# Kernel tuning notes

Hardware: AMD Instinct MI355X
Metric: run time of the kernel (lower is better)

The kernel has to match this reference:

```python
import jax, jax.numpy as jnp
import numpy as np
from jax import lax

EPS = 1e-5
DN = ('NCDHW', 'OIDHW', 'NCDHW')


def _instance_norm(x, w, b):
    # normalize over spatial dims per (batch, channel); biased variance like torch
    mu = jnp.mean(x, axis=(2, 3, 4), keepdims=True)
    var = jnp.mean((x - mu) ** 2, axis=(2, 3, 4), keepdims=True)
    xn = (x - mu) * lax.rsqrt(var + EPS)
    return xn * w[None, :, None, None, None] + b[None, :, None, None, None]


def _conv1x1(x, w, b):
    # w: [Cout, Cin]
    y = jnp.einsum('bcdhw,oc->bodhw', x, w)
    return y + b[None, :, None, None, None]


def _dwconv3(x, w, b):
    # depthwise 3x3x3, padding 1; w: [C, 1, 3, 3, 3]
    y = lax.conv_general_dilated(x, w, (1, 1, 1), 'SAME',
                                 dimension_numbers=DN,
                                 feature_group_count=w.shape[0])
    return y + b[None, :, None, None, None]


def setup_inputs() -> dict:
    key = jax.random.key(0)
    ks = jax.random.split(key, 8)
    C, half = 64, 32
    B, D, H, W = 1, 96, 96, 96
    s1 = 1.0 / np.sqrt(C)          # fan_in of 1x1 conv
    s3 = 1.0 / np.sqrt(27.0)       # fan_in of depthwise 3x3x3
    return {
        'x': jax.random.normal(ks[0], (B, C, D, H, W), jnp.float32),
        'norm_w': jnp.ones((C,), jnp.float32),
        'norm_b': jnp.zeros((C,), jnp.float32),
        'in_proj_w': jax.random.normal(ks[1], (C, C), jnp.float32) * s1,
        'in_proj_b': jnp.zeros((C,), jnp.float32),
        'conv_ssm_w': jax.random.normal(ks[2], (half, 1, 3, 3, 3), jnp.float32) * s3,
        'conv_ssm_b': jnp.zeros((half,), jnp.float32),
        'mamba_w': jax.random.normal(ks[3], (half, 1, 3, 3, 3), jnp.float32) * s3,
        'mamba_b': jnp.zeros((half,), jnp.float32),
        'conv_sym_w': jax.random.normal(ks[4], (half, 1, 3, 3, 3), jnp.float32) * s3,
        'conv_sym_b': jnp.zeros((half,), jnp.float32),
        'out_proj_w': jax.random.normal(ks[5], (C, C), jnp.float32) * s1,
        'out_proj_b': jnp.zeros((C,), jnp.float32),
    }


def reference(x, norm_w, norm_b, in_proj_w, in_proj_b,
              conv_ssm_w, conv_ssm_b, mamba_w, mamba_b,
              conv_sym_w, conv_sym_b, out_proj_w, out_proj_b):
    residual = x
    xp = _conv1x1(_instance_norm(x, norm_w, norm_b), in_proj_w, in_proj_b)
    half = xp.shape[1] // 2
    x1, x2 = xp[:, :half], xp[:, half:]
    # SSM branch (TriDirectionalMamba fallback = depthwise conv3)
    x1 = _dwconv3(jax.nn.silu(_dwconv3(x1, conv_ssm_w, conv_ssm_b)), mamba_w, mamba_b)
    # symmetric conv branch
    x2 = jax.nn.silu(_dwconv3(x2, conv_sym_w, conv_sym_b))
    y = _conv1x1(jnp.concatenate([x1, x2], axis=1), out_proj_w, out_proj_b)
    return y + residual
```

## Files before the change

### kernel.cpp

```cpp
#include <hip/hip_runtime.h>

typedef unsigned short u16;
typedef unsigned int u32;
typedef short bf16x8 __attribute__((ext_vector_type(8)));
typedef float f32x16 __attribute__((ext_vector_type(16)));
typedef u16 u16x8 __attribute__((ext_vector_type(8)));

#define DIM 96
#define PLANE (DIM*DIM)
#define S 884736
#define C 64
#define HALF 32
#define PARTS 16
#define EPS 1e-5f

#define RPAD 104
#define LROWS 18
#define LBUF (8 + LROWS*RPAD)

#define MFMA32(a,b,c) __builtin_amdgcn_mfma_f32_32x32x16_bf16(a,b,c,0,0,0)

__device__ __forceinline__ u16 f2bf(float f) {
  u32 u = __builtin_bit_cast(u32, f);
  return (u16)((u + 0x7FFFu + ((u >> 16) & 1u)) >> 16);
}
__device__ __forceinline__ float bf2f(u16 h) {
  return __builtin_bit_cast(float, (u32)h << 16);
}
__device__ __forceinline__ u32 cvt_pk_bf16(float lo, float hi) {
  u32 r;
  asm("v_cvt_pk_bf16_f32 %0, %1, %2" : "=v"(r) : "v"(lo), "v"(hi));
  return r;
}
__device__ __forceinline__ float silu(float v) { return v / (1.f + __expf(-v)); }
__device__ __forceinline__ u16x8 zero8() {
  u16x8 z;
  #pragma unroll
  for (int i = 0; i < 8; ++i) z[i] = 0;
  return z;
}

__global__ __launch_bounds__(256) void k1_stats(const float* __restrict__ x,
                                                u16* __restrict__ xb,
                                                float* __restrict__ psum,
                                                float* __restrict__ psq) {
  const int bid = blockIdx.x;
  const int ch = bid / PARTS, part = bid % PARTS;
  const int chunk = S / PARTS;
  const size_t base = (size_t)ch * S + (size_t)part * chunk;
  const float4* p = (const float4*)(x + base);
  ushort4* xb4 = (ushort4*)(xb + base);
  const int n4 = chunk / 4;
  float s = 0.f, q = 0.f;
  for (int i = threadIdx.x; i < n4; i += 256) {
    float4 v = p[i];
    s += (v.x + v.y) + (v.z + v.w);
    q += (v.x * v.x + v.y * v.y) + (v.z * v.z + v.w * v.w);
    union { u32 u[2]; ushort4 v4; } o;
    o.u[0] = cvt_pk_bf16(v.x, v.y);
    o.u[1] = cvt_pk_bf16(v.z, v.w);
    xb4[i] = o.v4;
  }
  #pragma unroll
  for (int off = 32; off > 0; off >>= 1) {
    s += __shfl_down(s, off);
    q += __shfl_down(q, off);
  }
  __shared__ float ls[4], lq[4];
  const int wid = threadIdx.x >> 6, lane = threadIdx.x & 63;
  if (lane == 0) { ls[wid] = s; lq[wid] = q; }
  __syncthreads();
  if (threadIdx.x == 0) {
    psum[bid] = (ls[0] + ls[1]) + (ls[2] + ls[3]);
    psq[bid]  = (lq[0] + lq[1]) + (lq[2] + lq[3]);
  }
}

__global__ __launch_bounds__(64) void k1b_prep(const float* __restrict__ psum,
    const float* __restrict__ psq,
    const float* __restrict__ norm_w, const float* __restrict__ norm_b,
    const float* __restrict__ in_w, const float* __restrict__ in_b,
    const float* __restrict__ out_w,
    u16* __restrict__ Wp, float* __restrict__ biasp, u16* __restrict__ Wo) {
  __shared__ float a_s[C], b2_s[C];
  const int t = threadIdx.x;
  float s = 0.f, q = 0.f;
  for (int i = 0; i < PARTS; ++i) { s += psum[t * PARTS + i]; q += psq[t * PARTS + i]; }
  const float inv = 1.f / (float)S;
  const float mu = s * inv;
  const float var = q * inv - mu * mu;
  const float rsig = rsqrtf(var + EPS);
  const float a = norm_w[t] * rsig;
  const float b2 = norm_b[t] - mu * a;
  a_s[t] = a; b2_s[t] = b2;
  __syncthreads();
  float bp = in_b[t];
  for (int c = 0; c < C; ++c) {
    const float w = in_w[t * C + c];
    Wp[t * C + c] = f2bf(w * a_s[c]);
    bp += b2_s[c] * w;
    Wo[t * C + c] = f2bf(out_w[t * C + c]);
  }
  biasp[t] = bp;
}

__global__ __launch_bounds__(256) void k2_mfma(const u16* __restrict__ xb,
    const u16* __restrict__ Wp, const float* __restrict__ biasp,
    u16* __restrict__ xp) {
  const int lane = threadIdx.x & 63, wid = threadIdx.x >> 6;
  const int n = lane & 31, hf = lane >> 5;
  const int v0 = blockIdx.x * 256 + wid * 64;
  bf16x8 A[2][4];
  #pragma unroll
  for (int t = 0; t < 2; ++t)
    #pragma unroll
    for (int s = 0; s < 4; ++s)
      A[t][s] = *(const bf16x8*)(Wp + (t * 32 + n) * C + s * 16 + hf * 8);

  f32x16 accE[2], accO[2];
  #pragma unroll
  for (int t = 0; t < 2; ++t)
    #pragma unroll
    for (int r = 0; r < 16; ++r) {
      const float b = biasp[t * 32 + (r & 3) + 8 * (r >> 2) + 4 * hf];
      accE[t][r] = b; accO[t][r] = b;
    }

  #pragma unroll
  for (int s = 0; s < 4; ++s) {
    union { u16 u[8]; bf16x8 v; } BE, BO;
    #pragma unroll
    for (int j = 0; j < 8; ++j) {
      const u32 xv = *(const u32*)(xb + (size_t)(s * 16 + hf * 8 + j) * S + v0 + 2 * n);
      BE.u[j] = (u16)(xv & 0xFFFFu); BO.u[j] = (u16)(xv >> 16);
    }
    #pragma unroll
    for (int t = 0; t < 2; ++t) {
      accE[t] = MFMA32(A[t][s], BE.v, accE[t]);
      accO[t] = MFMA32(A[t][s], BO.v, accO[t]);
    }
  }
  #pragma unroll
  for (int t = 0; t < 2; ++t)
    #pragma unroll
    for (int r = 0; r < 16; ++r) {
      const int o = t * 32 + (r & 3) + 8 * (r >> 2) + 4 * hf;
      *(u32*)(xp + (size_t)o * S + v0 + 2 * n) = cvt_pk_bf16(accE[t][r], accO[t][r]);
    }
}

__device__ __forceinline__ void fma3(float* __restrict__ a,
    const float* __restrict__ r, float t0, float t1, float t2) {
  #pragma unroll
  for (int i = 0; i < 8; ++i) a[i] = fmaf(t0, r[i], a[i]);
  #pragma unroll
  for (int i = 0; i < 8; ++i) a[i] = fmaf(t1, r[i + 1], a[i]);
  #pragma unroll
  for (int i = 0; i < 8; ++i) a[i] = fmaf(t2, r[i + 2], a[i]);
}

template<bool SILU, int DCHUNKT>
__global__ __launch_bounds__(192) void dwconv(const u16* __restrict__ srcA,
    const float* __restrict__ kwA, const float* __restrict__ bA,
    u16* __restrict__ dstA,
    const float* __restrict__ kwB, const float* __restrict__ bB,
    u16* __restrict__ dstB) {
  __shared__ u16 lds[2][LBUF];
  const int c = blockIdx.z;
  const u16* src = srcA + (size_t)c * S;
  u16* dst; const float* kwp; float bias;
  if (c < HALF) { dst = dstA + (size_t)c * S;          kwp = kwA + c * 27;          bias = bA[c]; }
  else          { dst = dstB + (size_t)(c - HALF) * S; kwp = kwB + (c - HALF) * 27; bias = bB[c - HALF]; }
  float kw[27];
  #pragma unroll
  for (int i = 0; i < 27; ++i) kw[i] = kwp[i];

  const int tx = threadIdx.x, ty = threadIdx.y;
  const int tid = ty * 12 + tx;
  const int w8 = tx * 8;
  const int h0 = blockIdx.x * 16;
  const int d0 = blockIdx.y * DCHUNKT;

  if (tid < 38) {
    const int b = tid / 19, k = tid % 19;
    *(u16x8*)&lds[b][RPAD * k] = zero8();
  }

  const int s_row0 = tid / 12, s_cc0 = tid % 12;
  const int s_row1 = (192 + tid) / 12, s_cc1 = (192 + tid) % 12;
  const bool has2 = tid < 24;
  const int s_h0 = h0 - 1 + s_row0;
  const int s_h1 = h0 - 1 + s_row1;
  const bool h0ok = (unsigned)s_h0 < DIM;
  const bool h1ok = has2 && ((unsigned)s_h1 < DIM);
  u16x8 vs0, vs1;

  #define STAGE_LOAD(DD) { \
    vs0 = zero8(); vs1 = zero8(); \
    if (((unsigned)(DD) < DIM) && h0ok) \
      vs0 = *(const u16x8*)(src + (size_t)(DD) * PLANE + s_h0 * DIM + s_cc0 * 8); \
    if (((unsigned)(DD) < DIM) && h1ok) \
      vs1 = *(const u16x8*)(src + (size_t)(DD) * PLANE + s_h1 * DIM + s_cc1 * 8); }

  #define STAGE_WRITE(WB) { \
    *(u16x8*)&lds[WB][8 + s_row0 * RPAD + s_cc0 * 8] = vs0; \
    if (has2) *(u16x8*)&lds[WB][8 + s_row1 * RPAD + s_cc1 * 8] = vs1; }

  float r0[10], r1[10], r2[10];
  float A[8], B[8], o8[8];

  #define LOADROW(R, ROWI, RB) { \
    const u16* _lb = &lds[RB][8 + (ROWI) * RPAD + w8]; \
    const u16x8 _m = *(const u16x8*)_lb; \
    const u16 _lo = _lb[-1], _hi = _lb[8]; \
    R[0] = bf2f(_lo); \
    _Pragma("unroll") \
    for (int i = 0; i < 8; ++i) R[1 + i] = bf2f(_m[i]); \
    R[9] = bf2f(_hi); }

  #define LOADROWS(RB) { LOADROW(r0, ty, RB); LOADROW(r1, ty + 1, RB); LOADROW(r2, ty + 2, RB); }

  #define CBLK(ACC, K0) { \
    fma3(ACC, r0, kw[(K0) + 0], kw[(K0) + 1], kw[(K0) + 2]); \
    fma3(ACC, r1, kw[(K0) + 3], kw[(K0) + 4], kw[(K0) + 5]); \
    fma3(ACC, r2, kw[(K0) + 6], kw[(K0) + 7], kw[(K0) + 8]); }

  STAGE_LOAD(d0 - 1);
  STAGE_WRITE(0);
  __syncthreads();

  LOADROWS(0);
  STAGE_LOAD(d0);
  #pragma unroll
  for (int i = 0; i < 8; ++i) B[i] = bias;
  CBLK(B, 0);
  STAGE_WRITE(1);
  __syncthreads();

  LOADROWS(1);
  STAGE_LOAD(d0 + 1);
  #pragma unroll
  for (int i = 0; i < 8; ++i) { A[i] = B[i]; B[i] = bias; }
  CBLK(A, 9);
  CBLK(B, 0);
  STAGE_WRITE(0);
  __syncthreads();

  u16* db = dst + (size_t)d0 * PLANE + (size_t)(h0 + ty) * DIM + w8;

  #define ROUND_BODY(D, RB, WB, DO_STG) { \
    LOADROWS(RB); \
    if (DO_STG) STAGE_LOAD((D) + 2); \
    _Pragma("unroll") \
    for (int i = 0; i < 8; ++i) o8[i] = A[i]; \
    CBLK(o8, 18); \
    _Pragma("unroll") \
    for (int i = 0; i < 8; ++i) A[i] = B[i]; \
    CBLK(A, 9); \
    _Pragma("unroll") \
    for (int i = 0; i < 8; ++i) B[i] = bias; \
    CBLK(B, 0); \
    if (SILU) { \
      _Pragma("unroll") \
      for (int i = 0; i < 8; ++i) o8[i] = silu(o8[i]); \
    } \
    union { u32 u[4]; u16x8 v; } _o; \
    _Pragma("unroll") \
    for (int i = 0; i < 4; ++i) _o.u[i] = cvt_pk_bf16(o8[2 * i], o8[2 * i + 1]); \
    *(u16x8*)db = _o.v; \
    db += PLANE; \
    if (DO_STG) STAGE_WRITE(WB); \
    __syncthreads(); }

  #pragma unroll 1
  for (int d = d0; d < d0 + DCHUNKT; d += 2) {
    ROUND_BODY(d, 0, 1, true);
    ROUND_BODY(d + 1, 1, 0, (d + 2) < d0 + DCHUNKT);
  }
  #undef ROUND_BODY
  #undef CBLK
  #undef LOADROWS
  #undef LOADROW
  #undef STAGE_WRITE
  #undef STAGE_LOAD
}

__global__ __launch_bounds__(256) void k4b_mfma(const u16* __restrict__ z_lo,
    const u16* __restrict__ z_hi, const u16* __restrict__ xb,
    const u16* __restrict__ Wo, const float* __restrict__ ob,
    float* __restrict__ out) {
  const int lane = threadIdx.x & 63, wid = threadIdx.x >> 6;
  const int n = lane & 31, hf = lane >> 5;
  const int v0 = blockIdx.x * 256 + wid * 64;
  bf16x8 A[2][4];
  #pragma unroll
  for (int t = 0; t < 2; ++t)
    #pragma unroll
    for (int s = 0; s < 4; ++s)
      A[t][s] = *(const bf16x8*)(Wo + (t * 32 + n) * C + s * 16 + hf * 8);

  f32x16 accE[2], accO[2];
  #pragma unroll
  for (int t = 0; t < 2; ++t)
    #pragma unroll
    for (int r = 0; r < 16; ++r) {
      const float b = ob[t * 32 + (r & 3) + 8 * (r >> 2) + 4 * hf];
      accE[t][r] = b; accO[t][r] = b;
    }

  #pragma unroll
  for (int s = 0; s < 4; ++s) {
    const u16* zbase = (s < 2) ? z_lo + (size_t)(s * 16) * S
                               : z_hi + (size_t)((s - 2) * 16) * S;
    union { u16 u[8]; bf16x8 v; } BE, BO;
    #pragma unroll
    for (int j = 0; j < 8; ++j) {
      const u32 zv = *(const u32*)(zbase + (size_t)(hf * 8 + j) * S + v0 + 2 * n);
      BE.u[j] = (u16)(zv & 0xFFFFu); BO.u[j] = (u16)(zv >> 16);
    }
    #pragma unroll
    for (int t = 0; t < 2; ++t) {
      accE[t] = MFMA32(A[t][s], BE.v, accE[t]);
      accO[t] = MFMA32(A[t][s], BO.v, accO[t]);
    }
  }
  #pragma unroll
  for (int t = 0; t < 2; ++t)
    #pragma unroll
    for (int r = 0; r < 16; ++r) {
      const int o = t * 32 + (r & 3) + 8 * (r >> 2) + 4 * hf;
      const u32 xr = *(const u32*)(xb + (size_t)o * S + v0 + 2 * n);
      float2 ov;
      ov.x = accE[t][r] + bf2f((u16)(xr & 0xFFFFu));
      ov.y = accO[t][r] + bf2f((u16)(xr >> 16));
      *(float2*)(out + (size_t)o * S + v0 + 2 * n) = ov;
    }
}

extern "C" void kernel_launch(void* const* d_in, const int* in_sizes, int n_in,
                              void* d_out, int out_size, void* d_ws, size_t ws_size,
                              hipStream_t stream) {
  const float* x      = (const float*)d_in[0];
  const float* norm_w = (const float*)d_in[1];
  const float* norm_b = (const float*)d_in[2];
  const float* in_w   = (const float*)d_in[3];
  const float* in_b   = (const float*)d_in[4];
  const float* ssm_w  = (const float*)d_in[5];
  const float* ssm_b  = (const float*)d_in[6];
  const float* mam_w  = (const float*)d_in[7];
  const float* mam_b  = (const float*)d_in[8];
  const float* sym_w  = (const float*)d_in[9];
  const float* sym_b  = (const float*)d_in[10];
  const float* out_w  = (const float*)d_in[11];
  const float* out_b  = (const float*)d_in[12];
  float* out = (float*)d_out;

  u16* xb   = (u16*)d_ws;
  u16* xp   = xb + (size_t)C * S;
  u16* t1   = xp + (size_t)C * S;
  u16* z_hi = t1 + (size_t)HALF * S;
  u16* z_lo = xp;
  float* psum  = (float*)(z_hi + (size_t)HALF * S);
  float* psq   = psum + C * PARTS;
  u16* Wp      = (u16*)(psq + C * PARTS);
  u16* Wo      = Wp + C * C;
  float* biasp = (float*)(Wo + C * C);

  k1_stats<<<C * PARTS, 256, 0, stream>>>(x, xb, psum, psq);
  k1b_prep<<<1, 64, 0, stream>>>(psum, psq, norm_w, norm_b, in_w, in_b, out_w,
                                 Wp, biasp, Wo);
  k2_mfma<<<S / 256, 256, 0, stream>>>(xb, Wp, biasp, xp);
  dwconv<true, 24><<<dim3(DIM / 16, 4, C), dim3(12, 16, 1), 0, stream>>>(
      xp, ssm_w, ssm_b, t1, sym_w, sym_b, z_hi);
  dwconv<false, 12><<<dim3(DIM / 16, 8, HALF), dim3(12, 16, 1), 0, stream>>>(
      t1, mam_w, mam_b, z_lo, mam_w, mam_b, z_lo);
  k4b_mfma<<<S / 256, 256, 0, stream>>>(z_lo, z_hi, xb, Wo, out_b, out);
}
```

Before: 353.3 us.

## Fuse back-to-back depthwise convolutions of SSM branch into one kernel

```diff
diff --git a/kernel.cpp b/kernel.cpp
--- a/kernel.cpp
+++ b/kernel.cpp
@@ -17,6 +17,7 @@
 #define RPAD 104
 #define LROWS 18
 #define LBUF (8 + LROWS*RPAD)
+#define FDCH 12
 
 #define MFMA32(a,b,c) __builtin_amdgcn_mfma_f32_32x32x16_bf16(a,b,c,0,0,0)
 
@@ -162,18 +163,16 @@
 template<bool SILU, int DCHUNKT>
 __global__ __launch_bounds__(192) void dwconv(const u16* __restrict__ srcA,
     const float* __restrict__ kwA, const float* __restrict__ bA,
-    u16* __restrict__ dstA,
-    const float* __restrict__ kwB, const float* __restrict__ bB,
-    u16* __restrict__ dstB) {
+    u16* __restrict__ dstA) {
   __shared__ u16 lds[2][LBUF];
   const int c = blockIdx.z;
   const u16* src = srcA + (size_t)c * S;
-  u16* dst; const float* kwp; float bias;
-  if (c < HALF) { dst = dstA + (size_t)c * S;          kwp = kwA + c * 27;          bias = bA[c]; }
-  else          { dst = dstB + (size_t)(c - HALF) * S; kwp = kwB + (c - HALF) * 27; bias = bB[c - HALF]; }
+  u16* dst = dstA + (size_t)c * S;
+  const float* kwp = kwA + c * 27;
   float kw[27];
   #pragma unroll
   for (int i = 0; i < 27; ++i) kw[i] = kwp[i];
+  const float bias = bA[c];
 
   const int tx = threadIdx.x, ty = threadIdx.y;
   const int tid = ty * 12 + tx;
@@ -283,6 +282,185 @@
   #undef LOADROW
   #undef STAGE_WRITE
   #undef STAGE_LOAD
+}
+
+__global__ __launch_bounds__(216) void fused_lo(const u16* __restrict__ xp,
+    const float* __restrict__ ssm_w, const float* __restrict__ ssm_b,
+    const float* __restrict__ mam_w, const float* __restrict__ mam_b,
+    u16* __restrict__ z_lo) {
+  __shared__ u16 inb[2][8 + 20 * RPAD];
+  __shared__ u16 tb[2][8 + 18 * RPAD];
+  const int c = blockIdx.z;
+  const u16* src = xp + (size_t)c * S;
+  u16* zdst = z_lo + (size_t)c * S;
+  float kw1[27], kw2[27];
+  #pragma unroll
+  for (int i = 0; i < 27; ++i) { kw1[i] = ssm_w[c * 27 + i]; kw2[i] = mam_w[c * 27 + i]; }
+  const float bias1 = ssm_b[c], bias2 = mam_b[c];
+
+  const int tx = threadIdx.x, ty = threadIdx.y;
+  const int tid = ty * 12 + tx;
+  const int w8 = tx * 8;
+  const int h0 = blockIdx.x * 16;
+  const int d0 = blockIdx.y * FDCH;
+
+  if (tid < 42) { *(u16x8*)&inb[tid / 21][(tid % 21) * RPAD] = zero8(); }
+  else if (tid < 80) { const int t2 = tid - 42; *(u16x8*)&tb[t2 / 19][(t2 % 19) * RPAD] = zero8(); }
+
+  const int s_row0 = ty, s_cc0 = tx;
+  const int s_row1 = 18 + tid / 12, s_cc1 = tid % 12;
+  const bool has2 = tid < 24;
+  const int gh0 = h0 - 2 + s_row0;
+  const int gh1 = h0 - 2 + s_row1;
+  const bool g0ok = (unsigned)gh0 < DIM;
+  const bool g1ok = has2 && ((unsigned)gh1 < DIM);
+  u16x8 vs0, vs1;
+
+  #define FS_LOAD(DD) { \
+    vs0 = zero8(); vs1 = zero8(); \
+    if (((unsigned)(DD) < DIM) && g0ok) \
+      vs0 = *(const u16x8*)(src + (size_t)(DD) * PLANE + gh0 * DIM + s_cc0 * 8); \
+    if (((unsigned)(DD) < DIM) && g1ok) \
+      vs1 = *(const u16x8*)(src + (size_t)(DD) * PLANE + gh1 * DIM + s_cc1 * 8); }
+
+  #define FS_WRITE(WB) { \
+    *(u16x8*)&inb[WB][8 + s_row0 * RPAD + s_cc0 * 8] = vs0; \
+    if (has2) *(u16x8*)&inb[WB][8 + s_row1 * RPAD + s_cc1 * 8] = vs1; }
+
+  const bool t1_h_ok = (unsigned)(h0 - 1 + ty) < DIM;
+  const bool zrole = ty < 16;
+  u16* zrow = zdst + (size_t)(h0 + ty) * DIM + w8;
+
+  float r0[10], r1[10], r2[10];
+  float A1[8], B1[8], A2[8], B2[8], o8[8];
+
+  #define FLOADROW(R, ROWI, BASE) { \
+    const u16* _lb = (BASE) + 8 + (ROWI) * RPAD + w8; \
+    const u16x8 _m = *(const u16x8*)_lb; \
+    const u16 _lo = _lb[-1], _hi = _lb[8]; \
+    R[0] = bf2f(_lo); \
+    _Pragma("unroll") \
+    for (int i = 0; i < 8; ++i) R[1 + i] = bf2f(_m[i]); \
+    R[9] = bf2f(_hi); }
+
+  #define FROWS(BASE) { FLOADROW(r0, ty, BASE); FLOADROW(r1, ty + 1, BASE); FLOADROW(r2, ty + 2, BASE); }
+
+  #define CBLKW(ACC, KW, K0) { \
+    fma3(ACC, r0, KW[(K0) + 0], KW[(K0) + 1], KW[(K0) + 2]); \
+    fma3(ACC, r1, KW[(K0) + 3], KW[(K0) + 4], KW[(K0) + 5]); \
+    fma3(ACC, r2, KW[(K0) + 6], KW[(K0) + 7], KW[(K0) + 8]); }
+
+  #define TEMIT(TT, TVAL) { \
+    union { u32 u[4]; u16x8 v; } _t; \
+    if (TVAL) { \
+      _Pragma("unroll") \
+      for (int i = 0; i < 8; ++i) o8[i] = silu(o8[i]); \
+      _Pragma("unroll") \
+      for (int i = 0; i < 4; ++i) _t.u[i] = cvt_pk_bf16(o8[2 * i], o8[2 * i + 1]); \
+    } else _t.v = zero8(); \
+    *(u16x8*)&tb[TT][8 + ty * RPAD + w8] = _t.v; }
+
+  FS_LOAD(d0 - 2);
+  FS_WRITE(0);
+  __syncthreads();
+
+  FS_LOAD(d0 - 1);
+  FROWS(inb[0]);
+  #pragma unroll
+  for (int i = 0; i < 8; ++i) B1[i] = bias1;
+  CBLKW(B1, kw1, 0);
+  FS_WRITE(1);
+  __syncthreads();
+
+  FS_LOAD(d0);
+  FROWS(inb[1]);
+  #pragma unroll
+  for (int i = 0; i < 8; ++i) { A1[i] = B1[i]; B1[i] = bias1; }
+  CBLKW(A1, kw1, 9);
+  CBLKW(B1, kw1, 0);
+  FS_WRITE(0);
+  __syncthreads();
+
+  FS_LOAD(d0 + 1);
+  FROWS(inb[0]);
+  #pragma unroll
+  for (int i = 0; i < 8; ++i) o8[i] = A1[i];
+  CBLKW(o8, kw1, 18);
+  #pragma unroll
+  for (int i = 0; i < 8; ++i) { A1[i] = B1[i]; B1[i] = bias1; }
+  CBLKW(A1, kw1, 9);
+  CBLKW(B1, kw1, 0);
+  { const bool tval = ((unsigned)(d0 - 1) < DIM) && t1_h_ok; TEMIT(1, tval); }
+  FS_WRITE(1);
+  __syncthreads();
+  if (zrole) {
+    FROWS(tb[1]);
+    #pragma unroll
+    for (int i = 0; i < 8; ++i) B2[i] = bias2;
+    CBLKW(B2, kw2, 0);
+  }
+
+  FS_LOAD(d0 + 2);
+  FROWS(inb[1]);
+  #pragma unroll
+  for (int i = 0; i < 8; ++i) o8[i] = A1[i];
+  CBLKW(o8, kw1, 18);
+  #pragma unroll
+  for (int i = 0; i < 8; ++i) { A1[i] = B1[i]; B1[i] = bias1; }
+  CBLKW(A1, kw1, 9);
+  CBLKW(B1, kw1, 0);
+  TEMIT(0, t1_h_ok);
+  FS_WRITE(0);
+  __syncthreads();
+  if (zrole) {
+    FROWS(tb[0]);
+    #pragma unroll
+    for (int i = 0; i < 8; ++i) { A2[i] = B2[i]; B2[i] = bias2; }
+    CBLKW(A2, kw2, 9);
+    CBLKW(B2, kw2, 0);
+  }
+
+  #define FSTEP(K, IB, TT) { \
+    const int jj = d0 - 2 + (K); \
+    if ((K) < FDCH + 3) FS_LOAD(jj + 1); \
+    FROWS(inb[IB]); \
+    _Pragma("unroll") \
+    for (int i = 0; i < 8; ++i) o8[i] = A1[i]; \
+    CBLKW(o8, kw1, 18); \
+    _Pragma("unroll") \
+    for (int i = 0; i < 8; ++i) { A1[i] = B1[i]; B1[i] = bias1; } \
+    CBLKW(A1, kw1, 9); \
+    CBLKW(B1, kw1, 0); \
+    { const bool tval = ((unsigned)(jj - 1) < DIM) && t1_h_ok; TEMIT(TT, tval); } \
+    if ((K) < FDCH + 3) FS_WRITE(IB ^ 1); \
+    __syncthreads(); \
+    if (zrole) { \
+      FROWS(tb[TT]); \
+      _Pragma("unroll") \
+      for (int i = 0; i < 8; ++i) o8[i] = A2[i]; \
+      CBLKW(o8, kw2, 18); \
+      _Pragma("unroll") \
+      for (int i = 0; i < 8; ++i) { A2[i] = B2[i]; B2[i] = bias2; } \
+      CBLKW(A2, kw2, 9); \
+      CBLKW(B2, kw2, 0); \
+      union { u32 u[4]; u16x8 v; } _z; \
+      _Pragma("unroll") \
+      for (int i = 0; i < 4; ++i) _z.u[i] = cvt_pk_bf16(o8[2 * i], o8[2 * i + 1]); \
+      *(u16x8*)(zrow + (size_t)(jj - 2) * PLANE) = _z.v; \
+    } }
+
+  #pragma unroll 1
+  for (int k = 4; k < FDCH + 4; k += 2) {
+    FSTEP(k, 0, 1);
+    FSTEP(k + 1, 1, 0);
+  }
+  #undef FSTEP
+  #undef TEMIT
+  #undef CBLKW
+  #undef FROWS
+  #undef FLOADROW
+  #undef FS_WRITE
+  #undef FS_LOAD
 }
 
 __global__ __launch_bounds__(256) void k4b_mfma(const u16* __restrict__ z_lo,
@@ -357,9 +535,8 @@
 
   u16* xb   = (u16*)d_ws;
   u16* xp   = xb + (size_t)C * S;
-  u16* t1   = xp + (size_t)C * S;
-  u16* z_hi = t1 + (size_t)HALF * S;
-  u16* z_lo = xp;
+  u16* z_lo = xp + (size_t)C * S;
+  u16* z_hi = z_lo + (size_t)HALF * S;
   float* psum  = (float*)(z_hi + (size_t)HALF * S);
   float* psq   = psum + C * PARTS;
   u16* Wp      = (u16*)(psq + C * PARTS);
@@ -370,9 +547,9 @@
   k1b_prep<<<1, 64, 0, stream>>>(psum, psq, norm_w, norm_b, in_w, in_b, out_w,
                                  Wp, biasp, Wo);
   k2_mfma<<<S / 256, 256, 0, stream>>>(xb, Wp, biasp, xp);
-  dwconv<true, 24><<<dim3(DIM / 16, 4, C), dim3(12, 16, 1), 0, stream>>>(
-      xp, ssm_w, ssm_b, t1, sym_w, sym_b, z_hi);
-  dwconv<false, 12><<<dim3(DIM / 16, 8, HALF), dim3(12, 16, 1), 0, stream>>>(
-      t1, mam_w, mam_b, z_lo, mam_w, mam_b, z_lo);
+  dwconv<true, 12><<<dim3(DIM / 16, 8, HALF), dim3(12, 16, 1), 0, stream>>>(
+      xp + (size_t)HALF * S, sym_w, sym_b, z_hi);
+  fused_lo<<<dim3(DIM / 16, DIM / FDCH, HALF), dim3(12, 18, 1), 0, stream>>>(
+      xp, ssm_w, ssm_b, mam_w, mam_b, z_lo);
   k4b_mfma<<<S / 256, 256, 0, stream>>>(z_lo, z_hi, xb, Wo, out_b, out);
 }
```

After: 372.5 us. 1.05x slower.
